# Kernel optimization log

Hardware: AMD Instinct MI355X
Metric: run time of the kernel (lower is better)

## Reference

```python
import jax, jax.numpy as jnp
import numpy as np

# ---- constants mirroring init_kwargs ----
S = 128          # sheet_units
KA = 25          # aff_cf_units
C = 2            # aff_cf_channels
KL = 25          # lat_cf_units
EXC = 9          # exc_units
DA = 1           # aff_cf_dilation
DL = 1           # lat_cf_dilation
HOMEO_TARGET = 0.04
STRENGTH = 1.0

# ---- radial helper masks (get_circle / get_radial_cos) ----
def _dist(n):
    g = jnp.arange(n, dtype=jnp.float32) - (n - 1) / 2.0
    return jnp.sqrt(g[:, None] ** 2 + g[None, :] ** 2)

def _circle(n, r):
    return (_dist(n) < r).astype(jnp.float32)

def _rcos(n, wl):
    return jnp.cos(_dist(n) * jnp.pi / wl)

# afferent envelope: [C*KA*KA], channel-major like torch repeat+view
_ae = _rcos(KA, KA) ** 2 * _circle(KA, KA / 2)
_ae = _ae / _ae.max()
AFF_ENV = jnp.tile(_ae.reshape(1, KA * KA), (C, 1)).reshape(C * KA * KA)

# lateral (LRI) envelope: [KL*KL]
_inh = _rcos(KL, EXC / DL) ** 2 * _circle(KL, EXC / (2 * DL))
_le = _rcos(KL, KL) ** 2 * (1.0 - _inh) * _circle(KL, KL / 2)
LRI_ENV = (_le / _le.max()).reshape(KL * KL)

def _unfold(x, k, dil):
    """x: [C,H,W] -> patches [L, C*k*k], torch F.unfold ordering (C slowest)."""
    Cc, H, W = x.shape
    out = H - dil * (k - 1)
    idx = jnp.arange(out)[:, None] + dil * jnp.arange(k)[None, :]  # [out,k]
    p = x[:, idx, :]          # [C,out,k,W]
    p = p[:, :, :, idx]       # [C,out,k,out,k]
    p = p.transpose(1, 3, 0, 2, 4)  # [out_i,out_j,C,ki,kj]
    return p.reshape(out * out, Cc * k * k)

def setup_inputs() -> dict:
    key = jax.random.key(0)
    k1, k2 = jax.random.split(key)
    in_size = S + DA * (KA - 1)  # 152
    x = jax.random.uniform(k1, (1, C, in_size, in_size), dtype=jnp.float32)
    rfs = jax.random.uniform(k2, (S * S, C * KA * KA, 1), dtype=jnp.float32)
    rfs = rfs / rfs.sum(1, keepdims=True)
    lat_weights = jnp.ones((S * S, KL * KL, 1), jnp.float32) / (KL * KL)
    adathresh = jnp.zeros((1, 1, S, S), jnp.float32)
    return {"x": x, "rfs": rfs, "lat_weights": lat_weights, "adathresh": adathresh}

def _forward(x, rfs, lat_weights, adathresh):
    relu = jax.nn.relu
    rfs = relu(rfs)                 # no_grad positive clamp of params
    lw = relu(lat_weights)
    # afferent: unfold + envelope + per-pixel dot (bmm with [L,F,1])
    tiles = _unfold(x[0], KA, DA) * AFF_ENV[None, :]          # [L, C*KA*KA]
    raw_aff = jnp.einsum('lf,lf->l', tiles, rfs[:, :, 0]).reshape(S, S)
    aff = jax.lax.stop_gradient(raw_aff) - adathresh[0, 0]
    lat = relu(aff)
    # lateral inhibition: pad so unfold yields S*S positions
    p = DL * (KL - 1) // 2
    lt = _unfold(jnp.pad(lat, p)[None], KL, DL) * LRI_ENV[None, :]  # [L, KL*KL]
    lat_neg = jnp.einsum('lf,lf->l', lt, jax.lax.stop_gradient(lw)[:, :, 0]).reshape(S, S)
    lat = lat - lat_neg
    lat = jnp.tanh(relu(lat * STRENGTH + aff))
    # hebbian lateral correlations term (learning_flag path)
    lt2 = _unfold(jnp.pad(lat, p, constant_values=HOMEO_TARGET)[None], KL, DL) * LRI_ENV[None, :]
    weighted = lt2 * lat.reshape(S * S, 1)
    lat_correlations = jnp.einsum('lf,lf->', weighted, lw[:, :, 0])
    return (raw_aff.reshape(1, 1, S, S), lat.reshape(1, 1, S, S),
            lat_correlations, tiles[:, None, :])

def reference(x, rfs, lat_weights, adathresh):
    return _forward(x, rfs, lat_weights, adathresh)
```

## Files before the change

### kernel.cpp

```cpp
#include <hip/hip_runtime.h>
#include <math.h>

#define S 128
#define KA 25
#define PATCH 625
#define FEAT 1250
#define PI_F 3.14159265358979323846f
#define PADW 152
#define PADA (PADW * PADW)

#define WS_LRI 0
#define WS_AE 640
#define WS_LAT0P 1280
#define WS_LATFP 24384
#define WS_PART 47488
#define NPART 4096

__device__ __forceinline__ int div25(int r) { return (r * 10486) >> 18; }
__device__ __forceinline__ int woff(int r) { return r + 127 * div25(r); }
__device__ __forceinline__ int eslot(int r) { return (r & 3) * 160 + (r >> 2); }

__device__ __forceinline__ void gld16(const float* g, float* l) {
    __builtin_amdgcn_global_load_lds(
        (const __attribute__((address_space(1))) void*)g,
        (__attribute__((address_space(3))) void*)l, 16, 0, 0);
}

__global__ __launch_bounds__(256) void k_init(float* __restrict__ ws) {
    const int tid = threadIdx.x;
    if (blockIdx.x == 0) {
        __shared__ float s_tmp[640];
        __shared__ float s_red[4];
        for (int s = tid; s < 640; s += 256) {
            int q = s / 160, t = s - q * 160;
            int r = (t << 2) | q;
            float v = 0.0f;
            if (r < PATCH) {
                float di = (float)div25(r) - 12.0f;
                float dj = (float)(r - 25 * div25(r)) - 12.0f;
                float d = sqrtf(di * di + dj * dj);
                if (d < 12.5f) {
                    float c = cosf(d * (PI_F / 25.0f));
                    v = c * c;
                }
            }
            ws[WS_AE + s] = v;
        }
        float m = 0.0f;
        for (int s = tid; s < 640; s += 256) {
            int q = s / 160, t = s - q * 160;
            int r = (t << 2) | q;
            float v = 0.0f;
            if (r < PATCH) {
                float di = (float)div25(r) - 12.0f;
                float dj = (float)(r - 25 * div25(r)) - 12.0f;
                float d = sqrtf(di * di + dj * dj);
                if (d < 12.5f) {
                    float c1 = cosf(d * (PI_F / 25.0f));
                    float inh = 0.0f;
                    if (d < 4.5f) {
                        float c2 = cosf(d * (PI_F / 9.0f));
                        inh = c2 * c2;
                    }
                    v = c1 * c1 * (1.0f - inh);
                }
            }
            s_tmp[s] = v;
            m = fmaxf(m, v);
        }
        for (int o = 32; o; o >>= 1) m = fmaxf(m, __shfl_down(m, o));
        if (!(tid & 63)) s_red[tid >> 6] = m;
        __syncthreads();
        float inv = 1.0f / fmaxf(fmaxf(s_red[0], s_red[1]),
                                 fmaxf(s_red[2], s_red[3]));
        for (int s = tid; s < 640; s += 256) ws[WS_LRI + s] = s_tmp[s] * inv;
    }
    const int gid = blockIdx.x * 256 + tid;
    const int gsz = gridDim.x * 256;
    for (int i = gid; i < 2 * PADA; i += gsz) {
        if (i < PADA) ws[WS_LAT0P + i] = 0.0f;
        else          ws[WS_LATFP + i - PADA] = 0.04f;
    }
}

__global__ __launch_bounds__(256) void k_afftiles(const float* __restrict__ x,
                                                  const float* __restrict__ rfs,
                                                  const float* __restrict__ ada,
                                                  float* __restrict__ raw_aff,
                                                  float* __restrict__ tiles,
                                                  float* __restrict__ ws) {
    __shared__ float s_ae[640];
    __shared__ float s_st[4 * 1280];
    const int tid = threadIdx.x;
    for (int i = tid; i < 640; i += 256) s_ae[i] = ws[WS_AE + i];
    __syncthreads();

    const int lane = tid & 63;
    const int wv = tid >> 6;
    const int l = blockIdx.x * 4 + wv;
    const int li = l >> 7, lj = l & 127;
    const int wb = li * PADW + lj;
    const long B = (long)l * FEAT;
    const int peel = (l & 1) ? 2 : 0;

    const float* gp = rfs + B + peel + 4 * lane;
    float* lp = s_st + wv * 1280;
#pragma unroll
    for (int i = 0; i < 4; ++i) gld16(gp + 256 * i, lp + 256 * i);
    if (lane < 56) gld16(gp + 1024, lp + 1024);

    float acc = 0.0f;
    if (lane < peel) {
        int f = lane;
        float t = x[wb + f] * s_ae[eslot(f)];
        tiles[B + f] = t;
        acc += t * fmaxf(rfs[B + f], 0.0f);
    }
    if (lane < 2 - peel) {
        int f = 1248 + lane;
        int r = f - PATCH;
        float t = x[PADA + wb + woff(r)] * s_ae[eslot(r)];
        tiles[B + f] = t;
        acc += t * fmaxf(rfs[B + f], 0.0f);
    }

    asm volatile("s_waitcnt vmcnt(0)" ::: "memory");
    __builtin_amdgcn_sched_barrier(0);

    auto consume = [&](int i) {
        const int k = i * 64 + lane;
        const float4 rv = *reinterpret_cast<const float4*>(lp + 4 * k);
        const int f0 = peel + 4 * k;
#pragma unroll
        for (int j = 0; j < 4; ++j) {
            int f = f0 + j;
            int c = (f >= PATCH) ? 1 : 0;
            int r = f - c * PATCH;
            float t = x[c * PADA + wb + woff(r)] * s_ae[eslot(r)];
            tiles[B + f] = t;
            acc += t * fmaxf((&rv.x)[j], 0.0f);
        }
    };
    consume(0); consume(1); consume(2); consume(3);
    if (lane < 56) consume(4);

    for (int o = 32; o; o >>= 1) acc += __shfl_down(acc, o);
    if (!lane) {
        raw_aff[l] = acc;
        ws[WS_LAT0P + (li + 12) * PADW + (lj + 12)] = fmaxf(acc - ada[l], 0.0f);
    }
}

__global__ __launch_bounds__(256) void k_lat(const float* __restrict__ raw_aff,
                                             const float* __restrict__ ada,
                                             const float* __restrict__ lw,
                                             float* __restrict__ latf,
                                             float* __restrict__ ws) {
    __shared__ float s_le[640];
    __shared__ float s_st[4 * 640];
    const int tid = threadIdx.x;
    for (int i = tid; i < 640; i += 256) s_le[i] = ws[WS_LRI + i];
    __syncthreads();

    const int lane = tid & 63;
    const int wv = tid >> 6;
    const int l = blockIdx.x * 4 + wv;
    const int li = l >> 7, lj = l & 127;
    const int wb = li * PADW + lj;
    const long B = (long)l * PATCH;
    const int peel = (4 - (l & 3)) & 3;
    const int n4 = (PATCH - peel) >> 2;
    const int rem = n4 - 128;
    const int tail = (PATCH - peel) & 3;
    const float* __restrict__ plat0 = ws + WS_LAT0P;

    const float* gp = lw + B + peel + 4 * lane;
    float* lp = s_st + wv * 640;
    gld16(gp, lp);
    gld16(gp + 256, lp + 256);
    if (lane < rem) gld16(gp + 512, lp + 512);

    float acc = 0.0f;
    if (lane < peel) {
        int f = lane;
        acc += plat0[wb + f] * s_le[eslot(f)] * fmaxf(lw[B + f], 0.0f);
    }
    if (lane < tail) {
        int f = peel + 4 * n4 + lane;
        acc += plat0[wb + woff(f)] * s_le[eslot(f)] * fmaxf(lw[B + f], 0.0f);
    }

    asm volatile("s_waitcnt vmcnt(0)" ::: "memory");
    __builtin_amdgcn_sched_barrier(0);

    auto consume = [&](int i) {
        const int k = i * 64 + lane;
        const float4 w4 = *reinterpret_cast<const float4*>(lp + 4 * k);
        const int f0 = peel + 4 * k;
#pragma unroll
        for (int j = 0; j < 4; ++j) {
            int f = f0 + j;
            acc += plat0[wb + woff(f)] * s_le[eslot(f)] * fmaxf((&w4.x)[j], 0.0f);
        }
    };
    consume(0); consume(1);
    if (lane < rem) consume(2);

    for (int o = 32; o; o >>= 1) acc += __shfl_down(acc, o);
    if (!lane) {
        float aff_l = raw_aff[l] - ada[l];
        float lat0_l = fmaxf(aff_l, 0.0f);
        float v = (lat0_l - acc)  + aff_l;
        float lv = tanhf(fmaxf(v, 0.0f));
        latf[l] = lv;
        ws[WS_LATFP + (li + 12) * PADW + (lj + 12)] = lv;
    }
}

__global__ __launch_bounds__(256) void k_corr(const float* __restrict__ latf,
                                              const float* __restrict__ lw,
                                              float* __restrict__ ws) {
    __shared__ float s_le[640];
    __shared__ float s_st[4 * 640];
    __shared__ float s_red[4];
    const int tid = threadIdx.x;
    for (int i = tid; i < 640; i += 256) s_le[i] = ws[WS_LRI + i];
    __syncthreads();

    const int lane = tid & 63, wv = tid >> 6;
    const int l = blockIdx.x * 4 + wv;
    const int li = l >> 7, lj = l & 127;
    const int wb = li * PADW + lj;
    const long B = (long)l * PATCH;
    const int peel = (4 - (l & 3)) & 3;
    const int n4 = (PATCH - peel) >> 2;
    const int rem = n4 - 128;
    const int tail = (PATCH - peel) & 3;
    const float* __restrict__ platf = ws + WS_LATFP;

    const float* gp = lw + B + peel + 4 * lane;
    float* lp = s_st + wv * 640;
    gld16(gp, lp);
    gld16(gp + 256, lp + 256);
    if (lane < rem) gld16(gp + 512, lp + 512);

    float acc = 0.0f;
    if (lane < peel) {
        int f = lane;
        acc += platf[wb + f] * s_le[eslot(f)] * fmaxf(lw[B + f], 0.0f);
    }
    if (lane < tail) {
        int f = peel + 4 * n4 + lane;
        acc += platf[wb + woff(f)] * s_le[eslot(f)] * fmaxf(lw[B + f], 0.0f);
    }

    asm volatile("s_waitcnt vmcnt(0)" ::: "memory");
    __builtin_amdgcn_sched_barrier(0);

    auto consume = [&](int i) {
        const int k = i * 64 + lane;
        const float4 w4 = *reinterpret_cast<const float4*>(lp + 4 * k);
        const int f0 = peel + 4 * k;
#pragma unroll
        for (int j = 0; j < 4; ++j) {
            int f = f0 + j;
            acc += platf[wb + woff(f)] * s_le[eslot(f)] * fmaxf((&w4.x)[j], 0.0f);
        }
    };
    consume(0); consume(1);
    if (lane < rem) consume(2);

    for (int o = 32; o; o >>= 1) acc += __shfl_down(acc, o);

    if (!lane) s_red[wv] = acc * latf[l];
    __syncthreads();
    if (!tid)
        ws[WS_PART + blockIdx.x] = s_red[0] + s_red[1] + s_red[2] + s_red[3];
}

__global__ __launch_bounds__(256) void k_reduce(const float* __restrict__ ws,
                                                float* __restrict__ corr) {
    __shared__ float s_red[4];
    const int tid = threadIdx.x;
    const int lane = tid & 63, wv = tid >> 6;
    float acc = 0.0f;
    for (int i = tid; i < NPART; i += 256) acc += ws[WS_PART + i];
    for (int o = 32; o; o >>= 1) acc += __shfl_down(acc, o);
    if (!lane) s_red[wv] = acc;
    __syncthreads();
    if (!tid) corr[0] = s_red[0] + s_red[1] + s_red[2] + s_red[3];
}

extern "C" void kernel_launch(void* const* d_in, const int* in_sizes, int n_in,
                              void* d_out, int out_size, void* d_ws, size_t ws_size,
                              hipStream_t stream) {
    const float* x   = (const float*)d_in[0];
    const float* rfs = (const float*)d_in[1];
    const float* lw  = (const float*)d_in[2];
    const float* ada = (const float*)d_in[3];

    float* out      = (float*)d_out;
    float* raw_aff  = out;
    float* latf     = out + S * S;
    float* corr     = out + 2 * S * S;
    float* tiles    = out + 2 * S * S + 1;
    float* ws       = (float*)d_ws;

    k_init<<<16, 256, 0, stream>>>(ws);
    k_afftiles<<<4096, 256, 0, stream>>>(x, rfs, ada, raw_aff, tiles, ws);
    k_lat<<<4096, 256, 0, stream>>>(raw_aff, ada, lw, latf, ws);
    k_corr<<<4096, 256, 0, stream>>>(latf, lw, ws);
    k_reduce<<<1, 256, 0, stream>>>(ws, corr);
}
```

Baseline: 227.4 us.

## Tile 16 pixels per block with LDS-staged input window and double-buffered weight streaming

Each block now covers 16 consecutive output pixels in one row (4 per wave) instead of 4 scattered pixels. It stages the shared input window (x, the padded lat0, or latf) into LDS once so the gathers read from LDS instead of global memory. Per-pixel weight rows are double-buffered with async global-to-LDS loads and explicit vmcnt waits, so the next pixel's loads overlap the current pixel's compute. The change also drops the permuted envelope layout, switches to scalar LDS reads, and cuts grid and partial counts from 4096 to 1024. The hand-tuned vmcnt counts are fragile, and the smaller grid exposes less parallelism.

```diff
diff --git a/kernel.cpp b/kernel.cpp
--- a/kernel.cpp
+++ b/kernel.cpp
@@ -14,66 +14,50 @@
 #define WS_LAT0P 1280
 #define WS_LATFP 24384
 #define WS_PART 47488
-#define NPART 4096
+#define NPART 1024
 
 __device__ __forceinline__ int div25(int r) { return (r * 10486) >> 18; }
-__device__ __forceinline__ int woff(int r) { return r + 127 * div25(r); }
-__device__ __forceinline__ int eslot(int r) { return (r & 3) * 160 + (r >> 2); }
 
 __device__ __forceinline__ void gld16(const float* g, float* l) {
     __builtin_amdgcn_global_load_lds(
         (const __attribute__((address_space(1))) void*)g,
         (__attribute__((address_space(3))) void*)l, 16, 0, 0);
 }
+#define VMCNT(N) asm volatile("s_waitcnt vmcnt(" #N ")" ::: "memory"); \
+                 __builtin_amdgcn_sched_barrier(0)
 
 __global__ __launch_bounds__(256) void k_init(float* __restrict__ ws) {
     const int tid = threadIdx.x;
     if (blockIdx.x == 0) {
         __shared__ float s_tmp[640];
         __shared__ float s_red[4];
-        for (int s = tid; s < 640; s += 256) {
-            int q = s / 160, t = s - q * 160;
-            int r = (t << 2) | q;
-            float v = 0.0f;
-            if (r < PATCH) {
-                float di = (float)div25(r) - 12.0f;
-                float dj = (float)(r - 25 * div25(r)) - 12.0f;
-                float d = sqrtf(di * di + dj * dj);
-                if (d < 12.5f) {
-                    float c = cosf(d * (PI_F / 25.0f));
-                    v = c * c;
+        float m = 0.0f;
+        for (int r = tid; r < PATCH; r += 256) {
+            int qi = div25(r);
+            float di = (float)qi - 12.0f;
+            float dj = (float)(r - 25 * qi) - 12.0f;
+            float d = sqrtf(di * di + dj * dj);
+            float ae = 0.0f, le = 0.0f;
+            if (d < 12.5f) {
+                float c1 = cosf(d * (PI_F / 25.0f));
+                ae = c1 * c1;
+                float inh = 0.0f;
+                if (d < 4.5f) {
+                    float c2 = cosf(d * (PI_F / 9.0f));
+                    inh = c2 * c2;
                 }
+                le = c1 * c1 * (1.0f - inh);
             }
-            ws[WS_AE + s] = v;
-        }
-        float m = 0.0f;
-        for (int s = tid; s < 640; s += 256) {
-            int q = s / 160, t = s - q * 160;
-            int r = (t << 2) | q;
-            float v = 0.0f;
-            if (r < PATCH) {
-                float di = (float)div25(r) - 12.0f;
-                float dj = (float)(r - 25 * div25(r)) - 12.0f;
-                float d = sqrtf(di * di + dj * dj);
-                if (d < 12.5f) {
-                    float c1 = cosf(d * (PI_F / 25.0f));
-                    float inh = 0.0f;
-                    if (d < 4.5f) {
-                        float c2 = cosf(d * (PI_F / 9.0f));
-                        inh = c2 * c2;
-                    }
-                    v = c1 * c1 * (1.0f - inh);
-                }
-            }
-            s_tmp[s] = v;
-            m = fmaxf(m, v);
+            ws[WS_AE + r] = ae;
+            s_tmp[r] = le;
+            m = fmaxf(m, le);
         }
         for (int o = 32; o; o >>= 1) m = fmaxf(m, __shfl_down(m, o));
         if (!(tid & 63)) s_red[tid >> 6] = m;
         __syncthreads();
         float inv = 1.0f / fmaxf(fmaxf(s_red[0], s_red[1]),
                                  fmaxf(s_red[2], s_red[3]));
-        for (int s = tid; s < 640; s += 256) ws[WS_LRI + s] = s_tmp[s] * inv;
+        for (int r = tid; r < PATCH; r += 256) ws[WS_LRI + r] = s_tmp[r] * inv;
     }
     const int gid = blockIdx.x * 256 + tid;
     const int gsz = gridDim.x * 256;
@@ -90,65 +74,99 @@
                                                   float* __restrict__ tiles,
                                                   float* __restrict__ ws) {
     __shared__ float s_ae[640];
-    __shared__ float s_st[4 * 1280];
-    const int tid = threadIdx.x;
-    for (int i = tid; i < 640; i += 256) s_ae[i] = ws[WS_AE + i];
+    __shared__ float s_x[2][25][40];
+    __shared__ float s_st[4][2][1280];
+    const int tid = threadIdx.x, lane = tid & 63, wv = tid >> 6;
+    const int blk = blockIdx.x;
+    const int li = blk >> 3;
+    const int lj0 = (blk & 7) << 4;
+
+    for (int i = tid; i < 625; i += 256) s_ae[i] = ws[WS_AE + i];
+    for (int i = tid; i < 2000; i += 256) {
+        int c = i >= 1000;
+        int rm = i - (c ? 1000 : 0);
+        int ki = rm / 40;
+        int col = rm - ki * 40;
+        s_x[c][ki][col] = x[c * PADA + (li + ki) * PADW + lj0 + col];
+    }
     __syncthreads();
 
-    const int lane = tid & 63;
-    const int wv = tid >> 6;
-    const int l = blockIdx.x * 4 + wv;
-    const int li = l >> 7, lj = l & 127;
-    const int wb = li * PADW + lj;
-    const long B = (long)l * FEAT;
-    const int peel = (l & 1) ? 2 : 0;
-
-    const float* gp = rfs + B + peel + 4 * lane;
-    float* lp = s_st + wv * 1280;
+    const int tc0 = wv << 2;
+    const int l0 = li * 128 + lj0 + tc0;
+
+    float acc_ht[4], ad[4];
+#define HT(n) { \
+        const int l = l0 + (n); const long B = (long)l * FEAT; \
+        const int peel = (l & 1) ? 2 : 0; \
+        float a = 0.0f; \
+        if (lane < 2) { \
+            int f = peel ? lane : (1248 + lane); \
+            int c = f >= 625; int r = f - (c ? 625 : 0); \
+            int ki = div25(r); int kj = r - 25 * ki; \
+            float t = s_x[c][ki][kj + tc0 + (n)] * s_ae[r]; \
+            tiles[B + f] = t; \
+            a = t * fmaxf(rfs[B + f], 0.0f); \
+        } \
+        if (!lane) ad[n] = ada[l]; \
+        acc_ht[n] = a; }
+    HT(0) HT(1) HT(2) HT(3)
+#undef HT
+
+    auto stage = [&](int n, float* buf) {
+        const int l = l0 + n;
+        const long B = (long)l * FEAT;
+        const int peel = (l & 1) ? 2 : 0;
+        const float* gp = rfs + B + peel + 4 * lane;
+        gld16(gp,        buf);
+        gld16(gp + 256,  buf + 256);
+        gld16(gp + 512,  buf + 512);
+        gld16(gp + 768,  buf + 768);
+        if (lane < 56) gld16(gp + 1024, buf + 1024);
+    };
+    auto consume = [&](int n, const float* buf, float accin, float adv) {
+        const int l = l0 + n;
+        const long B = (long)l * FEAT;
+        const int peel = (l & 1) ? 2 : 0;
+        const int tc = tc0 + n;
+        float acc = accin;
 #pragma unroll
-    for (int i = 0; i < 4; ++i) gld16(gp + 256 * i, lp + 256 * i);
-    if (lane < 56) gld16(gp + 1024, lp + 1024);
-
-    float acc = 0.0f;
-    if (lane < peel) {
-        int f = lane;
-        float t = x[wb + f] * s_ae[eslot(f)];
-        tiles[B + f] = t;
-        acc += t * fmaxf(rfs[B + f], 0.0f);
-    }
-    if (lane < 2 - peel) {
-        int f = 1248 + lane;
-        int r = f - PATCH;
-        float t = x[PADA + wb + woff(r)] * s_ae[eslot(r)];
-        tiles[B + f] = t;
-        acc += t * fmaxf(rfs[B + f], 0.0f);
-    }
-
-    asm volatile("s_waitcnt vmcnt(0)" ::: "memory");
+        for (int j = 0; j < 20; ++j) {
+            int fh = j * 64 + lane;
+            if (j < 19 || lane < 32) {
+                float rv = buf[fh];
+                int f = peel + fh;
+                int c = f >= 625;
+                int r = f - (c ? 625 : 0);
+                int ki = div25(r);
+                int kj = r - 25 * ki;
+                float t = s_x[c][ki][kj + tc] * s_ae[r];
+                tiles[B + f] = t;
+                acc += t * fmaxf(rv, 0.0f);
+            }
+        }
+        for (int o = 32; o; o >>= 1) acc += __shfl_down(acc, o);
+        if (!lane) {
+            raw_aff[l] = acc;
+            ws[WS_LAT0P + (li + 12) * PADW + lj0 + tc + 12] =
+                fmaxf(acc - adv, 0.0f);
+        }
+    };
+
+    float* buf0 = &s_st[wv][0][0];
+    float* buf1 = &s_st[wv][1][0];
     __builtin_amdgcn_sched_barrier(0);
-
-    auto consume = [&](int i) {
-        const int k = i * 64 + lane;
-        const float4 rv = *reinterpret_cast<const float4*>(lp + 4 * k);
-        const int f0 = peel + 4 * k;
-#pragma unroll
-        for (int j = 0; j < 4; ++j) {
-            int f = f0 + j;
-            int c = (f >= PATCH) ? 1 : 0;
-            int r = f - c * PATCH;
-            float t = x[c * PADA + wb + woff(r)] * s_ae[eslot(r)];
-            tiles[B + f] = t;
-            acc += t * fmaxf((&rv.x)[j], 0.0f);
-        }
-    };
-    consume(0); consume(1); consume(2); consume(3);
-    if (lane < 56) consume(4);
-
-    for (int o = 32; o; o >>= 1) acc += __shfl_down(acc, o);
-    if (!lane) {
-        raw_aff[l] = acc;
-        ws[WS_LAT0P + (li + 12) * PADW + (lj + 12)] = fmaxf(acc - ada[l], 0.0f);
-    }
+    stage(0, buf0);
+    stage(1, buf1);
+    VMCNT(5);
+    consume(0, buf0, acc_ht[0], ad[0]);
+    stage(2, buf0);
+    VMCNT(27);
+    consume(1, buf1, acc_ht[1], ad[1]);
+    stage(3, buf1);
+    VMCNT(27);
+    consume(2, buf0, acc_ht[2], ad[2]);
+    VMCNT(22);
+    consume(3, buf1, acc_ht[3], ad[3]);
 }
 
 __global__ __launch_bounds__(256) void k_lat(const float* __restrict__ raw_aff,
@@ -157,125 +175,195 @@
                                              float* __restrict__ latf,
                                              float* __restrict__ ws) {
     __shared__ float s_le[640];
-    __shared__ float s_st[4 * 640];
-    const int tid = threadIdx.x;
-    for (int i = tid; i < 640; i += 256) s_le[i] = ws[WS_LRI + i];
+    __shared__ float s_g[25][40];
+    __shared__ float s_st[4][2][640];
+    const int tid = threadIdx.x, lane = tid & 63, wv = tid >> 6;
+    const int blk = blockIdx.x;
+    const int li = blk >> 3;
+    const int lj0 = (blk & 7) << 4;
+
+    for (int i = tid; i < 625; i += 256) s_le[i] = ws[WS_LRI + i];
+    for (int i = tid; i < 1000; i += 256) {
+        int ki = i / 40;
+        int col = i - ki * 40;
+        s_g[ki][col] = ws[WS_LAT0P + (li + ki) * PADW + lj0 + col];
+    }
     __syncthreads();
 
-    const int lane = tid & 63;
-    const int wv = tid >> 6;
-    const int l = blockIdx.x * 4 + wv;
-    const int li = l >> 7, lj = l & 127;
-    const int wb = li * PADW + lj;
-    const long B = (long)l * PATCH;
-    const int peel = (4 - (l & 3)) & 3;
-    const int n4 = (PATCH - peel) >> 2;
-    const int rem = n4 - 128;
-    const int tail = (PATCH - peel) & 3;
-    const float* __restrict__ plat0 = ws + WS_LAT0P;
-
-    const float* gp = lw + B + peel + 4 * lane;
-    float* lp = s_st + wv * 640;
-    gld16(gp, lp);
-    gld16(gp + 256, lp + 256);
-    if (lane < rem) gld16(gp + 512, lp + 512);
-
-    float acc = 0.0f;
-    if (lane < peel) {
-        int f = lane;
-        acc += plat0[wb + f] * s_le[eslot(f)] * fmaxf(lw[B + f], 0.0f);
-    }
-    if (lane < tail) {
-        int f = peel + 4 * n4 + lane;
-        acc += plat0[wb + woff(f)] * s_le[eslot(f)] * fmaxf(lw[B + f], 0.0f);
-    }
-
-    asm volatile("s_waitcnt vmcnt(0)" ::: "memory");
+    const int tc0 = wv << 2;
+    const int l0 = li * 128 + lj0 + tc0;
+
+    float acc_ht[4], ra[4], ad[4];
+#define HT(n) { \
+        const int l = l0 + (n); const long B = (long)l * PATCH; \
+        const int peel = (4 - (l & 3)) & 3; \
+        const int fmax4 = (PATCH - peel) & ~3; \
+        const int tcnt = (PATCH - peel) & 3; \
+        float a = 0.0f; \
+        if (lane < peel) { \
+            int f = lane; int ki = div25(f); int kj = f - 25 * ki; \
+            a += s_g[ki][kj + tc0 + (n)] * s_le[f] * fmaxf(lw[B + f], 0.0f); \
+        } \
+        if (lane < tcnt) { \
+            int f = peel + fmax4 + lane; int ki = div25(f); int kj = f - 25 * ki; \
+            a += s_g[ki][kj + tc0 + (n)] * s_le[f] * fmaxf(lw[B + f], 0.0f); \
+        } \
+        if (!lane) { ra[n] = raw_aff[l]; ad[n] = ada[l]; } \
+        acc_ht[n] = a; }
+    HT(0) HT(1) HT(2) HT(3)
+#undef HT
+
+    auto stage = [&](int n, float* buf) {
+        const int l = l0 + n;
+        const long B = (long)l * PATCH;
+        const int peel = (4 - (l & 3)) & 3;
+        const int rem = ((PATCH - peel) >> 2) - 128;
+        const float* gp = lw + B + peel + 4 * lane;
+        gld16(gp,       buf);
+        gld16(gp + 256, buf + 256);
+        if (lane < rem) gld16(gp + 512, buf + 512);
+    };
+    auto consume = [&](int n, const float* buf, float accin, float rav,
+                       float adv) {
+        const int l = l0 + n;
+        const int peel = (4 - (l & 3)) & 3;
+        const int fmax4 = (PATCH - peel) & ~3;
+        const int tc = tc0 + n;
+        float acc = accin;
+#pragma unroll
+        for (int j = 0; j < 10; ++j) {
+            int fh = j * 64 + lane;
+            if (j < 9 || fh < fmax4) {
+                float wval = buf[fh];
+                int f = peel + fh;
+                int ki = div25(f);
+                int kj = f - 25 * ki;
+                acc += s_g[ki][kj + tc] * s_le[f] * fmaxf(wval, 0.0f);
+            }
+        }
+        for (int o = 32; o; o >>= 1) acc += __shfl_down(acc, o);
+        if (!lane) {
+            float aff_l = rav - adv;
+            float lat0_l = fmaxf(aff_l, 0.0f);
+            float v = (lat0_l - acc)  + aff_l;
+            float lv = tanhf(fmaxf(v, 0.0f));
+            latf[l] = lv;
+            ws[WS_LATFP + (li + 12) * PADW + lj0 + tc + 12] = lv;
+        }
+    };
+
+    float* buf0 = &s_st[wv][0][0];
+    float* buf1 = &s_st[wv][1][0];
     __builtin_amdgcn_sched_barrier(0);
-
-    auto consume = [&](int i) {
-        const int k = i * 64 + lane;
-        const float4 w4 = *reinterpret_cast<const float4*>(lp + 4 * k);
-        const int f0 = peel + 4 * k;
-#pragma unroll
-        for (int j = 0; j < 4; ++j) {
-            int f = f0 + j;
-            acc += plat0[wb + woff(f)] * s_le[eslot(f)] * fmaxf((&w4.x)[j], 0.0f);
-        }
-    };
-    consume(0); consume(1);
-    if (lane < rem) consume(2);
-
-    for (int o = 32; o; o >>= 1) acc += __shfl_down(acc, o);
-    if (!lane) {
-        float aff_l = raw_aff[l] - ada[l];
-        float lat0_l = fmaxf(aff_l, 0.0f);
-        float v = (lat0_l - acc)  + aff_l;
-        float lv = tanhf(fmaxf(v, 0.0f));
-        latf[l] = lv;
-        ws[WS_LATFP + (li + 12) * PADW + (lj + 12)] = lv;
-    }
+    stage(0, buf0);
+    stage(1, buf1);
+    VMCNT(3);
+    consume(0, buf0, acc_ht[0], ra[0], ad[0]);
+    stage(2, buf0);
+    VMCNT(5);
+    consume(1, buf1, acc_ht[1], ra[1], ad[1]);
+    stage(3, buf1);
+    VMCNT(5);
+    consume(2, buf0, acc_ht[2], ra[2], ad[2]);
+    VMCNT(2);
+    consume(3, buf1, acc_ht[3], ra[3], ad[3]);
 }
 
 __global__ __launch_bounds__(256) void k_corr(const float* __restrict__ latf,
                                               const float* __restrict__ lw,
                                               float* __restrict__ ws) {
     __shared__ float s_le[640];
-    __shared__ float s_st[4 * 640];
+    __shared__ float s_g[25][40];
+    __shared__ float s_st[4][2][640];
     __shared__ float s_red[4];
-    const int tid = threadIdx.x;
-    for (int i = tid; i < 640; i += 256) s_le[i] = ws[WS_LRI + i];
+    const int tid = threadIdx.x, lane = tid & 63, wv = tid >> 6;
+    const int blk = blockIdx.x;
+    const int li = blk >> 3;
+    const int lj0 = (blk & 7) << 4;
+
+    for (int i = tid; i < 625; i += 256) s_le[i] = ws[WS_LRI + i];
+    for (int i = tid; i < 1000; i += 256) {
+        int ki = i / 40;
+        int col = i - ki * 40;
+        s_g[ki][col] = ws[WS_LATFP + (li + ki) * PADW + lj0 + col];
+    }
     __syncthreads();
 
-    const int lane = tid & 63, wv = tid >> 6;
-    const int l = blockIdx.x * 4 + wv;
-    const int li = l >> 7, lj = l & 127;
-    const int wb = li * PADW + lj;
-    const long B = (long)l * PATCH;
-    const int peel = (4 - (l & 3)) & 3;
-    const int n4 = (PATCH - peel) >> 2;
-    const int rem = n4 - 128;
-    const int tail = (PATCH - peel) & 3;
-    const float* __restrict__ platf = ws + WS_LATFP;
-
-    const float* gp = lw + B + peel + 4 * lane;
-    float* lp = s_st + wv * 640;
-    gld16(gp, lp);
-    gld16(gp + 256, lp + 256);
-    if (lane < rem) gld16(gp + 512, lp + 512);
-
-    float acc = 0.0f;
-    if (lane < peel) {
-        int f = lane;
-        acc += platf[wb + f] * s_le[eslot(f)] * fmaxf(lw[B + f], 0.0f);
-    }
-    if (lane < tail) {
-        int f = peel + 4 * n4 + lane;
-        acc += platf[wb + woff(f)] * s_le[eslot(f)] * fmaxf(lw[B + f], 0.0f);
-    }
-
-    asm volatile("s_waitcnt vmcnt(0)" ::: "memory");
+    const int tc0 = wv << 2;
+    const int l0 = li * 128 + lj0 + tc0;
+
+    float acc_ht[4], lf[4];
+#define HT(n) { \
+        const int l = l0 + (n); const long B = (long)l * PATCH; \
+        const int peel = (4 - (l & 3)) & 3; \
+        const int fmax4 = (PATCH - peel) & ~3; \
+        const int tcnt = (PATCH - peel) & 3; \
+        float a = 0.0f; \
+        if (lane < peel) { \
+            int f = lane; int ki = div25(f); int kj = f - 25 * ki; \
+            a += s_g[ki][kj + tc0 + (n)] * s_le[f] * fmaxf(lw[B + f], 0.0f); \
+        } \
+        if (lane < tcnt) { \
+            int f = peel + fmax4 + lane; int ki = div25(f); int kj = f - 25 * ki; \
+            a += s_g[ki][kj + tc0 + (n)] * s_le[f] * fmaxf(lw[B + f], 0.0f); \
+        } \
+        if (!lane) lf[n] = latf[l]; \
+        acc_ht[n] = a; }
+    HT(0) HT(1) HT(2) HT(3)
+#undef HT
+
+    auto stage = [&](int n, float* buf) {
+        const int l = l0 + n;
+        const long B = (long)l * PATCH;
+        const int peel = (4 - (l & 3)) & 3;
+        const int rem = ((PATCH - peel) >> 2) - 128;
+        const float* gp = lw + B + peel + 4 * lane;
+        gld16(gp,       buf);
+        gld16(gp + 256, buf + 256);
+        if (lane < rem) gld16(gp + 512, buf + 512);
+    };
+    float wsum = 0.0f;
+    auto consume = [&](int n, const float* buf, float accin, float lfv) {
+        const int l = l0 + n;
+        const int peel = (4 - (l & 3)) & 3;
+        const int fmax4 = (PATCH - peel) & ~3;
+        const int tc = tc0 + n;
+        float acc = accin;
+#pragma unroll
+        for (int j = 0; j < 10; ++j) {
+            int fh = j * 64 + lane;
+            if (j < 9 || fh < fmax4) {
+                float wval = buf[fh];
+                int f = peel + fh;
+                int ki = div25(f);
+                int kj = f - 25 * ki;
+                acc += s_g[ki][kj + tc] * s_le[f] * fmaxf(wval, 0.0f);
+            }
+        }
+        for (int o = 32; o; o >>= 1) acc += __shfl_down(acc, o);
+        if (!lane) wsum += acc * lfv;
+    };
+
+    float* buf0 = &s_st[wv][0][0];
+    float* buf1 = &s_st[wv][1][0];
     __builtin_amdgcn_sched_barrier(0);
-
-    auto consume = [&](int i) {
-        const int k = i * 64 + lane;
-        const float4 w4 = *reinterpret_cast<const float4*>(lp + 4 * k);
-        const int f0 = peel + 4 * k;
-#pragma unroll
-        for (int j = 0; j < 4; ++j) {
-            int f = f0 + j;
-            acc += platf[wb + woff(f)] * s_le[eslot(f)] * fmaxf((&w4.x)[j], 0.0f);
-        }
-    };
-    consume(0); consume(1);
-    if (lane < rem) consume(2);
-
-    for (int o = 32; o; o >>= 1) acc += __shfl_down(acc, o);
-
-    if (!lane) s_red[wv] = acc * latf[l];
+    stage(0, buf0);
+    stage(1, buf1);
+    VMCNT(3);
+    consume(0, buf0, acc_ht[0], lf[0]);
+    stage(2, buf0);
+    VMCNT(3);
+    consume(1, buf1, acc_ht[1], lf[1]);
+    stage(3, buf1);
+    VMCNT(3);
+    consume(2, buf0, acc_ht[2], lf[2]);
+    VMCNT(0);
+    consume(3, buf1, acc_ht[3], lf[3]);
+
+    if (!lane) s_red[wv] = wsum;
     __syncthreads();
     if (!tid)
-        ws[WS_PART + blockIdx.x] = s_red[0] + s_red[1] + s_red[2] + s_red[3];
+        ws[WS_PART + blk] = s_red[0] + s_red[1] + s_red[2] + s_red[3];
 }
 
 __global__ __launch_bounds__(256) void k_reduce(const float* __restrict__ ws,
@@ -307,8 +395,8 @@
     float* ws       = (float*)d_ws;
 
     k_init<<<16, 256, 0, stream>>>(ws);
-    k_afftiles<<<4096, 256, 0, stream>>>(x, rfs, ada, raw_aff, tiles, ws);
-    k_lat<<<4096, 256, 0, stream>>>(raw_aff, ada, lw, latf, ws);
-    k_corr<<<4096, 256, 0, stream>>>(latf, lw, ws);
+    k_afftiles<<<1024, 256, 0, stream>>>(x, rfs, ada, raw_aff, tiles, ws);
+    k_lat<<<1024, 256, 0, stream>>>(raw_aff, ada, lw, latf, ws);
+    k_corr<<<1024, 256, 0, stream>>>(latf, lw, ws);
     k_reduce<<<1, 256, 0, stream>>>(ws, corr);
 }
```

Result: no change. 225.3 us (-0.9%).
